# Performance work log

Hardware: AMD Instinct MI355X
Metric: run time of the kernel (lower is better)

Reference implementation:

```python
import jax, jax.numpy as jnp
import numpy as np

DT_MIN, DT_MAX = 0.001, 0.1
CHUNK = 64


def setup_inputs() -> dict:
    key = jax.random.key(0)
    ks = jax.random.split(key, 8)
    b, L, D = 2, 4096, 1024
    d_inner, d_state, nheads, K = 2048, 128, 32, 4
    conv_dim = d_inner + 2 * d_state            # 2304
    d_in_proj = 2 * d_inner + 2 * d_state + nheads  # 4384
    f32 = jnp.float32
    return {
        'x': jax.random.normal(ks[0], (b, L, D), f32),
        'in_proj_w': jax.random.normal(ks[1], (d_in_proj, D), f32) * (D ** -0.5),
        'conv_w': jax.random.normal(ks[2], (conv_dim, K), f32) * 0.3,
        'conv_b': jnp.zeros((conv_dim,), f32),
        'dt_bias': jax.random.normal(ks[3], (nheads,), f32) * 0.5,
        'A_log': jnp.log(jax.random.uniform(ks[4], (nheads,), f32, 1.0, 16.0)),
        'D_skip': jnp.ones((nheads,), f32),
        'norm_w': jnp.ones((d_inner,), f32),
        'out_proj_w': jax.random.normal(ks[5], (D, d_inner), f32) * (d_inner ** -0.5),
        'ln_w': jnp.ones((D,), f32),
        'ln_b': jnp.zeros((D,), f32),
    }


def reference(x, in_proj_w, conv_w, conv_b, dt_bias, A_log, D_skip, norm_w, out_proj_w, ln_w, ln_b):
    b, L, d_model = x.shape
    d_inner = norm_w.shape[0]
    nheads = A_log.shape[0]
    hd = d_inner // nheads                      # headdim = 64
    conv_dim = conv_w.shape[0]
    d_state = (conv_dim - d_inner) // 2
    Q = CHUNK
    c = L // Q

    # ---- Mamba2 in_proj ----
    zxbcdt = jnp.einsum('bld,kd->blk', x, in_proj_w)
    z = zxbcdt[..., :d_inner]                                   # gate
    xBC = zxbcdt[..., d_inner:d_inner + conv_dim]
    dt_raw = zxbcdt[..., d_inner + conv_dim:]                   # (b,L,h)

    # ---- causal depthwise conv1d (kernel 4) + SiLU ----
    K = conv_w.shape[1]
    xp = jnp.pad(xBC, ((0, 0), (K - 1, 0), (0, 0)))
    conv = sum(xp[:, k:k + L, :] * conv_w[:, k] for k in range(K)) + conv_b
    xBC = jax.nn.silu(conv)
    x_ssm = xBC[..., :d_inner]
    Bm = xBC[..., d_inner:d_inner + d_state]                    # (b,L,n)
    Cm = xBC[..., d_inner + d_state:]                           # (b,L,n)

    # ---- bounded dt (sigmoid, per SSMBlock fix) ----
    dt = DT_MIN + (DT_MAX - DT_MIN) * jax.nn.sigmoid(dt_raw + dt_bias)  # (b,L,h)
    A = -jnp.exp(A_log)                                          # (h,)

    # ---- chunked SSD selective scan ----
    xh = x_ssm.reshape(b, c, Q, nheads, hd)
    dtc = dt.reshape(b, c, Q, nheads)
    x_dt = xh * dtc[..., None]
    dA = jnp.einsum('bcqh,h->bhcq', dtc, A)
    Acum = jnp.cumsum(dA, axis=-1)                               # (b,h,c,Q)
    Bc = Bm.reshape(b, c, Q, d_state)
    Cc = Cm.reshape(b, c, Q, d_state)

    # intra-chunk (diagonal blocks)
    seg = Acum[..., :, None] - Acum[..., None, :]                # (b,h,c,Q,Q)
    mask = jnp.tril(jnp.ones((Q, Q), bool))
    Lmat = jnp.exp(jnp.where(mask, seg, -jnp.inf))
    Yd = jnp.einsum('bcqn,bcsn,bhcqs,bcshp->bcqhp', Cc, Bc, Lmat, x_dt)

    # chunk end-states
    decay_states = jnp.exp(Acum[..., -1:] - Acum)                # (b,h,c,Q)
    states = jnp.einsum('bcqn,bhcq,bcqhp->bchpn', Bc, decay_states, x_dt)
    chunk_decay = jnp.exp(Acum[..., -1])                         # (b,h,c)

    def step(carry, inp):
        st, dec = inp
        return dec[..., None, None] * carry + st, carry

    _, prevs = jax.lax.scan(
        step, jnp.zeros((b, nheads, hd, d_state), x.dtype),
        (jnp.moveaxis(states, 1, 0), jnp.moveaxis(chunk_decay, 2, 0)))
    prevs = jnp.moveaxis(prevs, 0, 1)                            # (b,c,h,p,n)

    # inter-chunk contribution
    Yo = jnp.einsum('bcqn,bchpn,bhcq->bcqhp', Cc, prevs, jnp.exp(Acum))

    Y = (Yd + Yo).reshape(b, L, nheads, hd) + D_skip[None, None, :, None] * xh.reshape(b, L, nheads, hd)
    y = Y.reshape(b, L, d_inner)

    # ---- gated RMSNorm + out_proj ----
    y = y * jax.nn.silu(z)
    y = y * jax.lax.rsqrt(jnp.mean(y * y, axis=-1, keepdims=True) + 1e-5) * norm_w
    out = jnp.einsum('bli,di->bld', y, out_proj_w)

    # ---- SSMBlock: LayerNorm + (eval-mode dropout) + residual ----
    mu = jnp.mean(out, axis=-1, keepdims=True)
    var = jnp.mean((out - mu) ** 2, axis=-1, keepdims=True)
    ln = (out - mu) * jax.lax.rsqrt(var + 1e-5) * ln_w + ln_b
    return x + ln
```

## Files before the change

kernel.cpp:

```cpp
#include <hip/hip_runtime.h>
#include <math.h>

#define BSZ     2
#define LEN     4096
#define DMODEL  1024
#define DINNER  2048
#define DSTATE  128
#define NHEADS  32
#define HDIM    64
#define CONVDIM 2304
#define QC      64
#define NCHUNK  64
#define ROWS    (BSZ*LEN)
#define SDIM    (HDIM*DSTATE)
#define PB      136
#define PT      72
#define CGRP    (CONVDIM/8)

typedef __attribute__((ext_vector_type(8))) short short8;
typedef __attribute__((ext_vector_type(4))) float f32x4;

__device__ __forceinline__ float silu_(float x){ return x / (1.0f + expf(-x)); }
__device__ __forceinline__ float sigm_(float x){ return 1.0f / (1.0f + expf(-x)); }
__device__ __forceinline__ float bf2f(unsigned short u){
    return __uint_as_float(((unsigned int)u) << 16);
}
__device__ __forceinline__ unsigned short f2bf(float f){
    unsigned int u = __float_as_uint(f);
    u = (u + 0x7fffu + ((u >> 16) & 1u)) >> 16;
    return (unsigned short)u;
}

__device__ __forceinline__ int swzcol(int row, int col) {
    return ((((col >> 3) ^ (row >> 3)) & 7) << 3) | (col & 7);
}
__device__ __forceinline__ int swzblk(int row, int blk) {
    return (((blk ^ (row >> 3)) & 7) << 3);
}

__device__ __forceinline__ void gload16(const void* g, void* l) {
    __builtin_amdgcn_global_load_lds(
        (const __attribute__((address_space(1))) unsigned int*)g,
        (__attribute__((address_space(3))) unsigned int*)l, 16, 0, 0);
}

__global__ __launch_bounds__(256) void cast_bf16(const float* __restrict__ src,
                                                 unsigned short* __restrict__ dst,
                                                 int n4) {
    const int i = blockIdx.x * 256 + threadIdx.x;
    if (i >= n4) return;
    const float4 v = *(const float4*)(src + (size_t)i * 4);
    ushort4 o;
    o.x = f2bf(v.x); o.y = f2bf(v.y); o.z = f2bf(v.z); o.w = f2bf(v.w);
    *(ushort4*)(dst + (size_t)i * 4) = o;
}

template<bool BF16OUT>
__global__ __launch_bounds__(256) void gemm_bt_mfma(const unsigned short* __restrict__ A,
                                                    const unsigned short* __restrict__ B,
                                                    void* __restrict__ Cout,
                                                    int N, int K) {
    __shared__ unsigned short As[128 * 32];
    __shared__ unsigned short Bs[128 * 32];
    const int tid = threadIdx.x;
    const int wave = tid >> 6, lane = tid & 63;
    const int m0 = blockIdx.y * 128, n0 = blockIdx.x * 128;
    const int m_off = (wave >> 1) * 64, n_off = (wave & 1) * 64;

    f32x4 acc[4][4];
#pragma unroll
    for (int i = 0; i < 4; i++)
#pragma unroll
        for (int j = 0; j < 4; j++) acc[i][j] = (f32x4){0.f, 0.f, 0.f, 0.f};

    const int arow = m_off + (lane & 15);
    const int brow = n_off + (lane & 15);
    const int koff = (lane >> 4) * 16;

    for (int kt = 0; kt < K; kt += 32) {
#pragma unroll
        for (int u = 0; u < 2; u++) {
            const int f = u * 256 + tid;
            const int row = f >> 2;
            const int ke = (f & 3) * 8;
            gload16(A + (size_t)(m0 + row) * K + kt + ke, ((char*)As) + f * 16);
            gload16(B + (size_t)(n0 + row) * K + kt + ke, ((char*)Bs) + f * 16);
        }
        __syncthreads();
        short8 af[4], bfr[4];
#pragma unroll
        for (int i = 0; i < 4; i++)
            af[i] = *(const short8*)((const char*)As + (arow + i * 16) * 64 + koff);
#pragma unroll
        for (int j = 0; j < 4; j++)
            bfr[j] = *(const short8*)((const char*)Bs + (brow + j * 16) * 64 + koff);
#pragma unroll
        for (int i = 0; i < 4; i++)
#pragma unroll
            for (int j = 0; j < 4; j++)
                acc[i][j] = __builtin_amdgcn_mfma_f32_16x16x32_bf16(
                    af[i], bfr[j], acc[i][j], 0, 0, 0);
        __syncthreads();
    }

    const int crow = (lane >> 4) * 4;
    const int ccol = lane & 15;
#pragma unroll
    for (int i = 0; i < 4; i++)
#pragma unroll
        for (int j = 0; j < 4; j++) {
            const int n = n0 + n_off + j * 16 + ccol;
#pragma unroll
            for (int r = 0; r < 4; r++) {
                const int m = m0 + m_off + i * 16 + crow + r;
                if (BF16OUT)
                    ((unsigned short*)Cout)[(size_t)m * N + n] = f2bf(acc[i][j][r]);
                else
                    ((float*)Cout)[(size_t)m * N + n] = acc[i][j][r];
            }
        }
}

__global__ __launch_bounds__(256) void dtproj_mfma(const unsigned short* __restrict__ A,
                                                   const unsigned short* __restrict__ W,
                                                   const float* __restrict__ bias,
                                                   float* __restrict__ dtb,
                                                   int K) {
    __shared__ unsigned short As[128 * 32];
    __shared__ unsigned short Bs[32 * 32];
    const int tid = threadIdx.x;
    const int wave = tid >> 6, lane = tid & 63;
    const int quad = lane >> 4, l16 = lane & 15;
    const int m0 = blockIdx.x * 128;

    f32x4 acc[2][2];
#pragma unroll
    for (int i = 0; i < 2; i++)
#pragma unroll
        for (int j = 0; j < 2; j++) acc[i][j] = (f32x4){0.f, 0.f, 0.f, 0.f};

    for (int kt = 0; kt < K; kt += 32) {
#pragma unroll
        for (int u = 0; u < 2; u++) {
            const int f = u * 256 + tid;
            const int row = f >> 2, ke = (f & 3) * 8;
            gload16(A + (size_t)(m0 + row) * K + kt + ke, ((char*)As) + f * 16);
        }
        if (tid < 128) {
            const int row = tid >> 2, ke = (tid & 3) * 8;
            gload16(W + (size_t)row * K + kt + ke, ((char*)Bs) + tid * 16);
        }
        __syncthreads();
        short8 af[2], bfr[2];
#pragma unroll
        for (int i = 0; i < 2; i++)
            af[i] = *(const short8*)((const char*)As + (wave * 32 + i * 16 + l16) * 64 + quad * 16);
#pragma unroll
        for (int j = 0; j < 2; j++)
            bfr[j] = *(const short8*)((const char*)Bs + (j * 16 + l16) * 64 + quad * 16);
#pragma unroll
        for (int i = 0; i < 2; i++)
#pragma unroll
            for (int j = 0; j < 2; j++)
                acc[i][j] = __builtin_amdgcn_mfma_f32_16x16x32_bf16(
                    af[i], bfr[j], acc[i][j], 0, 0, 0);
        __syncthreads();
    }
#pragma unroll
    for (int i = 0; i < 2; i++)
#pragma unroll
        for (int j = 0; j < 2; j++) {
            const int h = j * 16 + l16;
            const float bh = bias[h];
#pragma unroll
            for (int r = 0; r < 4; r++) {
                const int m = m0 + wave * 32 + i * 16 + quad * 4 + r;
                dtb[(size_t)m * NHEADS + h] =
                    0.001f + 0.099f * sigm_(acc[i][j][r] + bh);
            }
        }
}

__global__ __launch_bounds__(256) void conv_silu_w(const unsigned short* __restrict__ xbc,
                                                   const float* __restrict__ cw,
                                                   const float* __restrict__ cb,
                                                   unsigned short* __restrict__ xssm,
                                                   unsigned short* __restrict__ Bb,
                                                   unsigned short* __restrict__ Cb) {
    const int idx = blockIdx.x * 256 + threadIdx.x;
    const int g = idx % CGRP;
    const int rowblk = idx / CGRP;
    const long row0 = (long)rowblk * 4;
    const int lbase = (int)(row0 & (LEN - 1));
    const int j0 = g * 8;

    float4 wv[8];
    float cbv[8];
#pragma unroll
    for (int e = 0; e < 8; e++) {
        wv[e] = *(const float4*)(cw + (size_t)(j0 + e) * 4);
        cbv[e] = cb[j0 + e];
    }

    short8 win[4];
    const short8 zero8 = (short8){0, 0, 0, 0, 0, 0, 0, 0};
#pragma unroll
    for (int t = 0; t < 3; t++) {
        const int lr = lbase - 3 + t;
        win[t] = (lr >= 0) ? *(const short8*)(xbc + (row0 - 3 + t) * CONVDIM + j0)
                           : zero8;
    }
#pragma unroll
    for (int i = 0; i < 4; i++) {
        win[3] = *(const short8*)(xbc + (row0 + i) * CONVDIM + j0);
        short8 o;
#pragma unroll
        for (int e = 0; e < 8; e++) {
            float acc = cbv[e];
            acc += bf2f((unsigned short)win[0][e]) * wv[e].x;
            acc += bf2f((unsigned short)win[1][e]) * wv[e].y;
            acc += bf2f((unsigned short)win[2][e]) * wv[e].z;
            acc += bf2f((unsigned short)win[3][e]) * wv[e].w;
            o[e] = (short)f2bf(silu_(acc));
        }
        const long row = row0 + i;
        if (j0 < DINNER)
            *(short8*)(xssm + row * DINNER + j0) = o;
        else if (j0 < DINNER + DSTATE)
            *(short8*)(Bb + row * DSTATE + (j0 - DINNER)) = o;
        else
            *(short8*)(Cb + row * DSTATE + (j0 - DINNER - DSTATE)) = o;
        win[0] = win[1]; win[1] = win[2]; win[2] = win[3];
    }
}

__global__ __launch_bounds__(64) void acum_kernel(const float* __restrict__ dtb,
                                                  const float* __restrict__ A_log,
                                                  float* __restrict__ Acum) {
    const int c = blockIdx.x, h = blockIdx.y, b = blockIdx.z;
    const int q = threadIdx.x;
    const float Av = -expf(A_log[h]);
    float v = dtb[((size_t)b * LEN + c * QC + q) * NHEADS + h] * Av;
#pragma unroll
    for (int off = 1; off < 64; off <<= 1) {
        const float n = __shfl_up(v, off, 64);
        if (q >= off) v += n;
    }
    Acum[(((size_t)b * NHEADS + h) * NCHUNK + c) * QC + q] = v;
}

__global__ __launch_bounds__(256) void chunk_mfma(const unsigned short* __restrict__ xssm,
                                                  const unsigned short* __restrict__ Bb,
                                                  const unsigned short* __restrict__ Cb,
                                                  const float* __restrict__ dtb,
                                                  const float* __restrict__ Acum,
                                                  const float* __restrict__ Dskip,
                                                  unsigned short* __restrict__ Y,
                                                  unsigned short* __restrict__ states) {
    const int c = blockIdx.x, h = blockIdx.y, b = blockIdx.z;
    const int tid = threadIdx.x;
    const int wave = tid >> 6, lane = tid & 63;
    const int quad = lane >> 4, l16 = lane & 15;

    __shared__ __attribute__((aligned(16))) unsigned short Bsh[8704];
    __shared__ __attribute__((aligned(16))) unsigned short Csh[9216];
    __shared__ __attribute__((aligned(16))) unsigned short xTs[4608];
    __shared__ float ac[QC], dts[QC], decs[QC];

    const size_t rowbase = (size_t)b * LEN + c * QC;
    if (tid < QC) {
        ac[tid]  = Acum[(((size_t)b * NHEADS + h) * NCHUNK + c) * QC + tid];
        dts[tid] = dtb[(rowbase + tid) * NHEADS + h];
    }
#pragma unroll
    for (int u = 0; u < 4; u++) {
        const int vi = u * 256 + tid;
        const int s = vi >> 4, n0 = (vi & 15) * 8;
        *(short8*)&Bsh[s * PB + n0] = *(const short8*)(Bb + (rowbase + s) * DSTATE + n0);
        *(short8*)&Csh[s * PB + n0] = *(const short8*)(Cb + (rowbase + s) * DSTATE + n0);
    }
#pragma unroll
    for (int u = 0; u < 2; u++) {
        const int vi = u * 256 + tid;
        const int q = vi >> 3, p0 = (vi & 7) * 8;
        const short8 v = *(const short8*)(xssm + (rowbase + q) * DINNER + h * HDIM + p0);
#pragma unroll
        for (int j = 0; j < 8; j++) {
            const int p = p0 + j;
            xTs[p * PT + swzcol(p, q)] = (unsigned short)v[j];
        }
    }
    __syncthreads();
    if (tid < QC) decs[tid] = expf(ac[QC - 1] - ac[tid]) * dts[tid];

    f32x4 S[4];
#pragma unroll
    for (int j = 0; j < 4; j++) S[j] = (f32x4){0.f, 0.f, 0.f, 0.f};
    const int qa = wave * 16 + l16;
#pragma unroll
    for (int ks = 0; ks < 4; ks++) {
        const short8 a = *(const short8*)&Csh[qa * PB + ks * 32 + quad * 8];
#pragma unroll
        for (int j = 0; j < 4; j++) {
            const short8 bb = *(const short8*)&Bsh[(j * 16 + l16) * PB + ks * 32 + quad * 8];
            S[j] = __builtin_amdgcn_mfma_f32_16x16x32_bf16(a, bb, S[j], 0, 0, 0);
        }
    }
    unsigned short slv[4][4];
#pragma unroll
    for (int j = 0; j < 4; j++)
#pragma unroll
        for (int r = 0; r < 4; r++) {
            const int q = wave * 16 + quad * 4 + r, s = j * 16 + l16;
            const float v = (s <= q) ? S[j][r] * expf(ac[q] - ac[s]) * dts[s] : 0.f;
            slv[j][r] = f2bf(v);
        }
    __syncthreads();

    {
        const int sin = lane & 7;
        const int ng  = lane >> 3;
#pragma unroll
        for (int so = 0; so < 2; so++) {
            const int s = (wave * 2 + so) * 8 + sin;
            const float d = decs[s];
            const int cb = s >> 3;
#pragma unroll
            for (int nh = 0; nh < 2; nh++) {
                const int noct = ng + 8 * nh;
                const int colphys = (((cb ^ noct) & 7) << 3) | (s & 7);
#pragma unroll
                for (int j = 0; j < 8; j++) {
                    const int n = noct * 8 + ((j + sin) & 7);
                    Csh[n * PT + colphys] = f2bf(bf2f(Bsh[s * PB + n]) * d);
                }
            }
        }
    }
    __syncthreads();

#pragma unroll
    for (int j = 0; j < 4; j++)
#pragma unroll
        for (int r = 0; r < 4; r++) {
            const int row = wave * 16 + quad * 4 + r;
            const int col = j * 16 + l16;
            Bsh[row * PT + swzcol(row, col)] = slv[j][r];
        }
    __syncthreads();

    f32x4 yd[4];
#pragma unroll
    for (int j = 0; j < 4; j++) yd[j] = (f32x4){0.f, 0.f, 0.f, 0.f};
#pragma unroll
    for (int ks = 0; ks < 2; ks++) {
        const int blk = ks * 4 + quad;
        const short8 a = *(const short8*)&Bsh[qa * PT + swzblk(qa, blk)];
#pragma unroll
        for (int j = 0; j < 4; j++) {
            const int row = j * 16 + l16;
            const short8 xb = *(const short8*)&xTs[row * PT + swzblk(row, blk)];
            yd[j] = __builtin_amdgcn_mfma_f32_16x16x32_bf16(a, xb, yd[j], 0, 0, 0);
        }
    }
    const float Dh = Dskip[h];
#pragma unroll
    for (int j = 0; j < 4; j++)
#pragma unroll
        for (int r = 0; r < 4; r++) {
            const int q = wave * 16 + quad * 4 + r, p = j * 16 + l16;
            const float v = yd[j][r] + Dh * bf2f(xTs[p * PT + swzcol(p, q)]);
            Y[(rowbase + q) * DINNER + h * HDIM + p] = f2bf(v);
        }

    f32x4 st[8];
#pragma unroll
    for (int j = 0; j < 8; j++) st[j] = (f32x4){0.f, 0.f, 0.f, 0.f};
#pragma unroll
    for (int ks = 0; ks < 2; ks++) {
        const int blk = ks * 4 + quad;
        const short8 a = *(const short8*)&xTs[qa * PT + swzblk(qa, blk)];
#pragma unroll
        for (int j = 0; j < 8; j++) {
            const int row = j * 16 + l16;
            const short8 bb = *(const short8*)&Csh[row * PT + swzblk(row, blk)];
            st[j] = __builtin_amdgcn_mfma_f32_16x16x32_bf16(a, bb, st[j], 0, 0, 0);
        }
    }
    const size_t sbase = (((size_t)b * NHEADS + h) * NCHUNK + c) * SDIM;
#pragma unroll
    for (int j = 0; j < 8; j++)
#pragma unroll
        for (int r = 0; r < 4; r++) {
            const int p = wave * 16 + quad * 4 + r, n = j * 16 + l16;
            states[sbase + (size_t)p * DSTATE + n] = f2bf(st[j][r]);
        }
}

__global__ __launch_bounds__(256) void scan_kernel(unsigned short* __restrict__ states,
                                                   const float* __restrict__ Acum) {
    __shared__ float dec[NCHUNK];
    const int bh = blockIdx.y;
    const int pn = blockIdx.x * 256 + threadIdx.x;
    if (threadIdx.x < NCHUNK)
        dec[threadIdx.x] = expf(Acum[((size_t)bh * NCHUNK + threadIdx.x) * QC + (QC - 1)]);
    __syncthreads();
    float carry = 0.f;
    const size_t base = (size_t)bh * NCHUNK * SDIM + pn;
    for (int c = 0; c < NCHUNK; c++) {
        const size_t idx = base + (size_t)c * SDIM;
        const float s = bf2f(states[idx]);
        states[idx] = f2bf(carry);
        carry = dec[c] * carry + s;
    }
}

__global__ __launch_bounds__(256) void yo_mfma(const unsigned short* __restrict__ Cb,
                                               const unsigned short* __restrict__ prevs,
                                               const float* __restrict__ Acum,
                                               unsigned short* __restrict__ Y) {
    const int c = blockIdx.x, h = blockIdx.y, b = blockIdx.z;
    const int tid = threadIdx.x;
    const int wave = tid >> 6, lane = tid & 63;
    const int quad = lane >> 4, l16 = lane & 15;
    __shared__ __attribute__((aligned(16))) unsigned short Csh[8704];
    __shared__ __attribute__((aligned(16))) unsigned short Psh[8704];
    __shared__ float eq[QC];
    const size_t rowbase = (size_t)b * LEN + c * QC;
    const size_t pbase = (((size_t)b * NHEADS + h) * NCHUNK + c) * SDIM;
    if (tid < QC)
        eq[tid] = expf(Acum[(((size_t)b * NHEADS + h) * NCHUNK + c) * QC + tid]);
#pragma unroll
    for (int u = 0; u < 4; u++) {
        const int vi = u * 256 + tid;
        const int r = vi >> 4, n0 = (vi & 15) * 8;
        *(short8*)&Csh[r * PB + n0] = *(const short8*)(Cb + (rowbase + r) * DSTATE + n0);
        *(short8*)&Psh[r * PB + n0] = *(const short8*)(prevs + pbase + (size_t)r * DSTATE + n0);
    }
    __syncthreads();

    f32x4 acc[4];
#pragma unroll
    for (int j = 0; j < 4; j++) acc[j] = (f32x4){0.f, 0.f, 0.f, 0.f};
    const int qa = wave * 16 + l16;
#pragma unroll
    for (int ks = 0; ks < 4; ks++) {
        const short8 a = *(const short8*)&Csh[qa * PB + ks * 32 + quad * 8];
#pragma unroll
        for (int j = 0; j < 4; j++) {
            const short8 bb = *(const short8*)&Psh[(j * 16 + l16) * PB + ks * 32 + quad * 8];
            acc[j] = __builtin_amdgcn_mfma_f32_16x16x32_bf16(a, bb, acc[j], 0, 0, 0);
        }
    }
#pragma unroll
    for (int j = 0; j < 4; j++)
#pragma unroll
        for (int r = 0; r < 4; r++) {
            const int q = wave * 16 + quad * 4 + r, p = j * 16 + l16;
            const size_t off = (rowbase + q) * DINNER + h * HDIM + p;
            Y[off] = f2bf(bf2f(Y[off]) + eq[q] * acc[j][r]);
        }
}

__global__ __launch_bounds__(256) void gate_rms(const unsigned short* __restrict__ Y,
                                                const unsigned short* __restrict__ zbf,
                                                const float* __restrict__ nw,
                                                unsigned short* __restrict__ ybf) {
    const int r = blockIdx.x, tid = threadIdx.x;
    float4 yv[2];
    float ss = 0.f;
#pragma unroll
    for (int u = 0; u < 2; u++) {
        const int col = u * 1024 + tid * 4;
        const ushort4 y4 = *(const ushort4*)(Y + (size_t)r * DINNER + col);
        const ushort4 z4 = *(const ushort4*)(zbf + (size_t)r * DINNER + col);
        float4 y;
        y.x = bf2f(y4.x) * silu_(bf2f(z4.x)); y.y = bf2f(y4.y) * silu_(bf2f(z4.y));
        y.z = bf2f(y4.z) * silu_(bf2f(z4.z)); y.w = bf2f(y4.w) * silu_(bf2f(z4.w));
        yv[u] = y;
        ss += y.x * y.x + y.y * y.y + y.z * y.z + y.w * y.w;
    }
#pragma unroll
    for (int off = 32; off; off >>= 1) ss += __shfl_xor(ss, off, 64);
    __shared__ float red[4];
    if ((tid & 63) == 0) red[tid >> 6] = ss;
    __syncthreads();
    ss = red[0] + red[1] + red[2] + red[3];
    const float scale = rsqrtf(ss / (float)DINNER + 1e-5f);
#pragma unroll
    for (int u = 0; u < 2; u++) {
        const int col = u * 1024 + tid * 4;
        const float4 w4 = *(const float4*)(nw + col);
        ushort4 o;
        o.x = f2bf(yv[u].x * scale * w4.x); o.y = f2bf(yv[u].y * scale * w4.y);
        o.z = f2bf(yv[u].z * scale * w4.z); o.w = f2bf(yv[u].w * scale * w4.w);
        *(ushort4*)(ybf + (size_t)r * DINNER + col) = o;
    }
}

__global__ __launch_bounds__(256) void ln_res(const float* __restrict__ outb,
                                              const float* __restrict__ x,
                                              const float* __restrict__ lw,
                                              const float* __restrict__ lb,
                                              float* __restrict__ out) {
    const int r = blockIdx.x, tid = threadIdx.x;
    const int col = tid * 4;
    const float4 v = *(const float4*)(outb + (size_t)r * DMODEL + col);
    float s = v.x + v.y + v.z + v.w;
    float s2 = v.x * v.x + v.y * v.y + v.z * v.z + v.w * v.w;
#pragma unroll
    for (int off = 32; off; off >>= 1) {
        s += __shfl_xor(s, off, 64);
        s2 += __shfl_xor(s2, off, 64);
    }
    __shared__ float rs[4], rs2[4];
    if ((tid & 63) == 0) { rs[tid >> 6] = s; rs2[tid >> 6] = s2; }
    __syncthreads();
    s = rs[0] + rs[1] + rs[2] + rs[3];
    s2 = rs2[0] + rs2[1] + rs2[2] + rs2[3];
    const float mu = s / (float)DMODEL;
    const float var = s2 / (float)DMODEL - mu * mu;
    const float inv = rsqrtf(var + 1e-5f);
    const float4 xw = *(const float4*)(x + (size_t)r * DMODEL + col);
    const float4 w4 = *(const float4*)(lw + col);
    const float4 b4 = *(const float4*)(lb + col);
    float4 o;
    o.x = xw.x + (v.x - mu) * inv * w4.x + b4.x;
    o.y = xw.y + (v.y - mu) * inv * w4.y + b4.y;
    o.z = xw.z + (v.z - mu) * inv * w4.z + b4.z;
    o.w = xw.w + (v.w - mu) * inv * w4.w + b4.w;
    *(float4*)(out + (size_t)r * DMODEL + col) = o;
}

extern "C" void kernel_launch(void* const* d_in, const int* in_sizes, int n_in,
                              void* d_out, int out_size, void* d_ws, size_t ws_size,
                              hipStream_t stream) {
    const float* x          = (const float*)d_in[0];
    const float* in_proj_w  = (const float*)d_in[1];
    const float* conv_w     = (const float*)d_in[2];
    const float* conv_b     = (const float*)d_in[3];
    const float* dt_bias    = (const float*)d_in[4];
    const float* A_log      = (const float*)d_in[5];
    const float* D_skip     = (const float*)d_in[6];
    const float* norm_w     = (const float*)d_in[7];
    const float* out_proj_w = (const float*)d_in[8];
    const float* ln_w       = (const float*)d_in[9];
    const float* ln_b       = (const float*)d_in[10];
    float* out = (float*)d_out;
    float* ws = (float*)d_ws;

    size_t off = 0;
    unsigned short* zbf     = (unsigned short*)(ws + off); off += (size_t)ROWS * DINNER / 2;
    unsigned short* xssm_bf = (unsigned short*)(ws + off); off += (size_t)ROWS * DINNER / 2;
    unsigned short* uni     = (unsigned short*)(ws + off); off += (size_t)ROWS * CONVDIM / 2;
    unsigned short* Bb_bf   = (unsigned short*)(ws + off); off += (size_t)ROWS * DSTATE / 2;
    unsigned short* Cb_bf   = (unsigned short*)(ws + off); off += (size_t)ROWS * DSTATE / 2;
    float* dtb   = ws + off; off += (size_t)ROWS * NHEADS;
    float* Acum  = ws + off; off += (size_t)BSZ * NHEADS * NCHUNK * QC;
    unsigned short* x_bf  = (unsigned short*)(ws + off); off += (size_t)ROWS * DMODEL / 2;
    unsigned short* wi_bf = (unsigned short*)(ws + off); off += (size_t)4384 * DMODEL / 2;
    unsigned short* wo_bf = (unsigned short*)(ws + off); off += (size_t)DMODEL * DINNER / 2;
    unsigned short* states = (unsigned short*)(ws + off); off += (size_t)BSZ * NHEADS * NCHUNK * SDIM / 2;
    const size_t need_bytes = off * sizeof(float);
    if (ws_size < need_bytes) return;

    unsigned short* xbc_bf = uni;
    unsigned short* Ybf    = uni;
    unsigned short* ybf    = xssm_bf;

    cast_bf16<<<(ROWS * DMODEL / 4 + 255) / 256, 256, 0, stream>>>(x, x_bf, ROWS * DMODEL / 4);
    cast_bf16<<<(4384 * DMODEL / 4 + 255) / 256, 256, 0, stream>>>(in_proj_w, wi_bf, 4384 * DMODEL / 4);
    cast_bf16<<<(DMODEL * DINNER / 4 + 255) / 256, 256, 0, stream>>>(out_proj_w, wo_bf, DMODEL * DINNER / 4);

    gemm_bt_mfma<true><<<dim3(DINNER / 128, ROWS / 128), 256, 0, stream>>>(
        x_bf, wi_bf, zbf, DINNER, DMODEL);
    gemm_bt_mfma<true><<<dim3(CONVDIM / 128, ROWS / 128), 256, 0, stream>>>(
        x_bf, wi_bf + (size_t)DINNER * DMODEL, xbc_bf, CONVDIM, DMODEL);
    dtproj_mfma<<<ROWS / 128, 256, 0, stream>>>(
        x_bf, wi_bf + (size_t)(DINNER + CONVDIM) * DMODEL, dt_bias, dtb, DMODEL);

    conv_silu_w<<<(ROWS / 4) * CGRP / 256, 256, 0, stream>>>(
        xbc_bf, conv_w, conv_b, xssm_bf, Bb_bf, Cb_bf);
    acum_kernel<<<dim3(NCHUNK, NHEADS, BSZ), 64, 0, stream>>>(dtb, A_log, Acum);
    chunk_mfma<<<dim3(NCHUNK, NHEADS, BSZ), 256, 0, stream>>>(
        xssm_bf, Bb_bf, Cb_bf, dtb, Acum, D_skip, Ybf, states);
    scan_kernel<<<dim3(SDIM / 256, BSZ * NHEADS), 256, 0, stream>>>(states, Acum);
    yo_mfma<<<dim3(NCHUNK, NHEADS, BSZ), 256, 0, stream>>>(Cb_bf, states, Acum, Ybf);
    gate_rms<<<ROWS, 256, 0, stream>>>(Ybf, zbf, norm_w, ybf);

    gemm_bt_mfma<false><<<dim3(DMODEL / 128, ROWS / 128), 256, 0, stream>>>(
        ybf, wo_bf, out, DMODEL, DINNER);
    ln_res<<<ROWS, 256, 0, stream>>>(out, x, ln_w, ln_b, out);
}
```

Before: 457.1 us.

## Replace GEMM with 256x256-tile double-buffered 8-wave pipelined MFMA kernel

Replaces the simple 128x128 single-buffered bf16 GEMM with a 512-thread kernel that computes 256x256 output tiles over a K-step of 64. It double-buffers LDS, staging the next tile's quarters while issuing MFMAs on the current one, and orders the work with explicit vmcnt/lgkmcnt waits and barriers. It also XOR-swizzles LDS columns to avoid bank conflicts, remaps block IDs across XCDs for L2 locality, and raises MFMA wave priority. The aim is to hide global load latency and raise arithmetic intensity, at the cost of heavy register and LDS use (128KB LDS) and fragile hand-tuned wait counts. The 2304-wide conv GEMM divides evenly into 256-wide tiles (9 tiles).

```diff
diff --git a/kernel.cpp b/kernel.cpp
--- a/kernel.cpp
+++ b/kernel.cpp
@@ -55,70 +55,143 @@
     *(ushort4*)(dst + (size_t)i * 4) = o;
 }
 
+__device__ __forceinline__ void stage_half(const unsigned short* __restrict__ G,
+                                           void* ldsbase, int w, int lane,
+                                           size_t rowbase, int K, int kt) {
+#pragma unroll
+    for (int u = 0; u < 2; u++) {
+        const int f = w * 128 + u * 64 + lane;
+        const int r = f >> 3;
+        const int cl = (lane & 7) ^ (lane >> 3);
+        gload16(G + rowbase + (size_t)r * K + kt + cl * 8,
+                (char*)ldsbase + f * 16);
+    }
+}
+
+#define WAITV(n) asm volatile("s_waitcnt vmcnt(" #n ")" ::: "memory")
+#define LGKM0    asm volatile("s_waitcnt lgkmcnt(0)" ::: "memory")
+#define BARRIER  do { asm volatile("" ::: "memory"); \
+                      __builtin_amdgcn_s_barrier();  \
+                      asm volatile("" ::: "memory"); } while (0)
+
+#define READ_A(dst, half)                                                     \
+    _Pragma("unroll")                                                         \
+    for (int fr = 0; fr < 4; fr++) {                                          \
+        const int r_ = (w & 1) * 64 + fr * 16 + l16;                          \
+        _Pragma("unroll")                                                     \
+        for (int s = 0; s < 2; s++)                                           \
+            dst[fr][s] = *(const short8*)((const char*)&lds[cb][0][half][0]   \
+                + r_ * 128 + (((s * 4 + quad) ^ rx7) << 4));                  \
+    }
+#define READ_B(dst, half)                                                     \
+    _Pragma("unroll")                                                         \
+    for (int fc = 0; fc < 2; fc++) {                                          \
+        const int r_ = (w >> 1) * 32 + fc * 16 + l16;                         \
+        _Pragma("unroll")                                                     \
+        for (int s = 0; s < 2; s++)                                           \
+            dst[fc][s] = *(const short8*)((const char*)&lds[cb][1][half][0]   \
+                + r_ * 128 + (((s * 4 + quad) ^ rx7) << 4));                  \
+    }
+#define MFMA16(g, af, bfv)                                                    \
+    __builtin_amdgcn_s_setprio(1);                                            \
+    _Pragma("unroll")                                                         \
+    for (int s = 0; s < 2; s++)                                               \
+        _Pragma("unroll")                                                     \
+        for (int fr = 0; fr < 4; fr++)                                        \
+            _Pragma("unroll")                                                 \
+            for (int fc = 0; fc < 2; fc++)                                    \
+                acc[g][fr][fc] = __builtin_amdgcn_mfma_f32_16x16x32_bf16(     \
+                    af[fr][s], bfv[fc][s], acc[g][fr][fc], 0, 0, 0);          \
+    __builtin_amdgcn_s_setprio(0);
+
 template<bool BF16OUT>
-__global__ __launch_bounds__(256) void gemm_bt_mfma(const unsigned short* __restrict__ A,
-                                                    const unsigned short* __restrict__ B,
-                                                    void* __restrict__ Cout,
-                                                    int N, int K) {
-    __shared__ unsigned short As[128 * 32];
-    __shared__ unsigned short Bs[128 * 32];
+__global__ __launch_bounds__(512, 2) void gemm8p(const unsigned short* __restrict__ A,
+                                                 const unsigned short* __restrict__ B,
+                                                 void* __restrict__ Cout,
+                                                 int N, int K, int gx) {
+    __shared__ unsigned short lds[2][2][2][8192];
     const int tid = threadIdx.x;
-    const int wave = tid >> 6, lane = tid & 63;
-    const int m0 = blockIdx.y * 128, n0 = blockIdx.x * 128;
-    const int m_off = (wave >> 1) * 64, n_off = (wave & 1) * 64;
-
-    f32x4 acc[4][4];
-#pragma unroll
-    for (int i = 0; i < 4; i++)
-#pragma unroll
-        for (int j = 0; j < 4; j++) acc[i][j] = (f32x4){0.f, 0.f, 0.f, 0.f};
-
-    const int arow = m_off + (lane & 15);
-    const int brow = n_off + (lane & 15);
-    const int koff = (lane >> 4) * 16;
-
-    for (int kt = 0; kt < K; kt += 32) {
-#pragma unroll
-        for (int u = 0; u < 2; u++) {
-            const int f = u * 256 + tid;
-            const int row = f >> 2;
-            const int ke = (f & 3) * 8;
-            gload16(A + (size_t)(m0 + row) * K + kt + ke, ((char*)As) + f * 16);
-            gload16(B + (size_t)(n0 + row) * K + kt + ke, ((char*)Bs) + f * 16);
-        }
-        __syncthreads();
-        short8 af[4], bfr[4];
+    const int w = tid >> 6, lane = tid & 63;
+    const int quad = lane >> 4, l16 = lane & 15;
+    const int rx7 = l16 & 7;
+
+    const int nwg = gridDim.x;
+    const int id = blockIdx.x;
+    const int q8 = nwg >> 3, r8 = nwg & 7;
+    const int xcd = id & 7, idx = id >> 3;
+    const int wg = (xcd < r8 ? xcd * (q8 + 1) : r8 * (q8 + 1) + (xcd - r8) * q8) + idx;
+    const int m0 = (wg / gx) * 256, n0 = (wg % gx) * 256;
+
+    f32x4 acc[4][4][2];
+#pragma unroll
+    for (int g = 0; g < 4; g++)
 #pragma unroll
         for (int i = 0; i < 4; i++)
-            af[i] = *(const short8*)((const char*)As + (arow + i * 16) * 64 + koff);
-#pragma unroll
-        for (int j = 0; j < 4; j++)
-            bfr[j] = *(const short8*)((const char*)Bs + (brow + j * 16) * 64 + koff);
-#pragma unroll
-        for (int i = 0; i < 4; i++)
-#pragma unroll
-            for (int j = 0; j < 4; j++)
-                acc[i][j] = __builtin_amdgcn_mfma_f32_16x16x32_bf16(
-                    af[i], bfr[j], acc[i][j], 0, 0, 0);
-        __syncthreads();
-    }
-
-    const int crow = (lane >> 4) * 4;
-    const int ccol = lane & 15;
-#pragma unroll
-    for (int i = 0; i < 4; i++)
-#pragma unroll
-        for (int j = 0; j < 4; j++) {
-            const int n = n0 + n_off + j * 16 + ccol;
-#pragma unroll
-            for (int r = 0; r < 4; r++) {
-                const int m = m0 + m_off + i * 16 + crow + r;
-                if (BF16OUT)
-                    ((unsigned short*)Cout)[(size_t)m * N + n] = f2bf(acc[i][j][r]);
-                else
-                    ((float*)Cout)[(size_t)m * N + n] = acc[i][j][r];
+#pragma unroll
+            for (int j = 0; j < 2; j++) acc[g][i][j] = (f32x4){0.f, 0.f, 0.f, 0.f};
+
+    const int NT = K >> 6;
+    stage_half(A, &lds[0][0][0][0], w, lane, (size_t)m0 * K, K, 0);
+    stage_half(B, &lds[0][1][0][0], w, lane, (size_t)n0 * K, K, 0);
+    stage_half(A, &lds[0][0][1][0], w, lane, (size_t)(m0 + 128) * K, K, 0);
+    stage_half(B, &lds[0][1][1][0], w, lane, (size_t)(n0 + 128) * K, K, 0);
+    WAITV(4); BARRIER;
+
+    short8 af0[4][2], af1[4][2], bf0[2][2], bf1[2][2];
+    int cb = 0;
+    for (int t = 0; t < NT - 1; t++) {
+        const int kn = (t + 1) * 64;
+        const int nb = cb ^ 1;
+        READ_A(af0, 0); READ_B(bf0, 0);
+        stage_half(A, &lds[nb][0][0][0], w, lane, (size_t)m0 * K, K, kn);
+        WAITV(4); BARRIER;
+        MFMA16(0, af0, bf0);
+        LGKM0; BARRIER;
+        READ_A(af1, 1);
+        stage_half(B, &lds[nb][1][0][0], w, lane, (size_t)n0 * K, K, kn);
+        WAITV(4); BARRIER;
+        MFMA16(1, af1, bf0);
+        LGKM0; BARRIER;
+        READ_B(bf1, 1);
+        stage_half(A, &lds[nb][0][1][0], w, lane, (size_t)(m0 + 128) * K, K, kn);
+        WAITV(6); BARRIER;
+        MFMA16(2, af0, bf1);
+        LGKM0; BARRIER;
+        stage_half(B, &lds[nb][1][1][0], w, lane, (size_t)(n0 + 128) * K, K, kn);
+        WAITV(4); BARRIER;
+        MFMA16(3, af1, bf1);
+        LGKM0; BARRIER;
+        cb = nb;
+    }
+    WAITV(0); BARRIER;
+    READ_A(af0, 0); READ_B(bf0, 0);
+    MFMA16(0, af0, bf0);
+    READ_A(af1, 1);
+    MFMA16(1, af1, bf0);
+    READ_B(bf1, 1);
+    MFMA16(2, af0, bf1);
+    MFMA16(3, af1, bf1);
+
+#pragma unroll
+    for (int g = 0; g < 4; g++) {
+        const int qm = g & 1, qn = g >> 1;
+        const int mb = m0 + qm * 128 + (w & 1) * 64;
+        const int nb2 = n0 + qn * 128 + (w >> 1) * 32;
+#pragma unroll
+        for (int fr = 0; fr < 4; fr++)
+#pragma unroll
+            for (int fc = 0; fc < 2; fc++) {
+                const int n = nb2 + fc * 16 + l16;
+#pragma unroll
+                for (int rr = 0; rr < 4; rr++) {
+                    const int m = mb + fr * 16 + quad * 4 + rr;
+                    if (BF16OUT)
+                        ((unsigned short*)Cout)[(size_t)m * N + n] = f2bf(acc[g][fr][fc][rr]);
+                    else
+                        ((float*)Cout)[(size_t)m * N + n] = acc[g][fr][fc][rr];
+                }
             }
-        }
+    }
 }
 
 __global__ __launch_bounds__(256) void dtproj_mfma(const unsigned short* __restrict__ A,
@@ -324,11 +397,11 @@
         for (int so = 0; so < 2; so++) {
             const int s = (wave * 2 + so) * 8 + sin;
             const float d = decs[s];
-            const int cb = s >> 3;
+            const int cbk = s >> 3;
 #pragma unroll
             for (int nh = 0; nh < 2; nh++) {
                 const int noct = ng + 8 * nh;
-                const int colphys = (((cb ^ noct) & 7) << 3) | (s & 7);
+                const int colphys = (((cbk ^ noct) & 7) << 3) | (s & 7);
 #pragma unroll
                 for (int j = 0; j < 8; j++) {
                     const int n = noct * 8 + ((j + sin) & 7);
@@ -572,10 +645,10 @@
     cast_bf16<<<(4384 * DMODEL / 4 + 255) / 256, 256, 0, stream>>>(in_proj_w, wi_bf, 4384 * DMODEL / 4);
     cast_bf16<<<(DMODEL * DINNER / 4 + 255) / 256, 256, 0, stream>>>(out_proj_w, wo_bf, DMODEL * DINNER / 4);
 
-    gemm_bt_mfma<true><<<dim3(DINNER / 128, ROWS / 128), 256, 0, stream>>>(
-        x_bf, wi_bf, zbf, DINNER, DMODEL);
-    gemm_bt_mfma<true><<<dim3(CONVDIM / 128, ROWS / 128), 256, 0, stream>>>(
-        x_bf, wi_bf + (size_t)DINNER * DMODEL, xbc_bf, CONVDIM, DMODEL);
+    gemm8p<true><<<(ROWS / 256) * (DINNER / 256), 512, 0, stream>>>(
+        x_bf, wi_bf, zbf, DINNER, DMODEL, DINNER / 256);
+    gemm8p<true><<<(ROWS / 256) * (CONVDIM / 256), 512, 0, stream>>>(
+        x_bf, wi_bf + (size_t)DINNER * DMODEL, xbc_bf, CONVDIM, DMODEL, CONVDIM / 256);
     dtproj_mfma<<<ROWS / 128, 256, 0, stream>>>(
         x_bf, wi_bf + (size_t)(DINNER + CONVDIM) * DMODEL, dt_bias, dtb, DMODEL);
 
@@ -588,7 +661,7 @@
     yo_mfma<<<dim3(NCHUNK, NHEADS, BSZ), 256, 0, stream>>>(Cb_bf, states, Acum, Ybf);
     gate_rms<<<ROWS, 256, 0, stream>>>(Ybf, zbf, norm_w, ybf);
 
-    gemm_bt_mfma<false><<<dim3(DMODEL / 128, ROWS / 128), 256, 0, stream>>>(
-        ybf, wo_bf, out, DMODEL, DINNER);
+    gemm8p<false><<<(ROWS / 256) * (DMODEL / 256), 512, 0, stream>>>(
+        ybf, wo_bf, out, DMODEL, DINNER, DMODEL / 256);
     ln_res<<<ROWS, 256, 0, stream>>>(out, x, ln_w, ln_b, out);
 }
```

After: 428.3 us. 6.3% less time.
